# Performance work log

Hardware: AMD Instinct MI355X
Metric: run time of the kernel (lower is better)

Reference implementation:

```python
import jax, jax.numpy as jnp
import numpy as np

L, B, E = 2048, 4, 512      # seq len (= MoE group dim), batch (= MoE tokens-per-group), embed
H = 8                        # attention heads
FF = 2048                    # expert hidden dim
NE = 5                       # num experts
EPS = 1e-9
THRESHOLD = 0.2              # second_threshold_eval
CAP_FACTOR = 2.0             # capacity_factor_eval
MIN_CAP = 4
CAP = max(min(B, int(B * 2 * CAP_FACTOR / NE)), MIN_CAP)  # expert capacity per group


def setup_inputs() -> dict:
    key = jax.random.key(0)
    ks = jax.random.split(key, 8)
    s = lambda k, shape, scale: jax.random.normal(k, shape, jnp.float32) * scale
    return {
        "x": s(ks[0], (L, B, E), 1.0),
        "ln1_w": jnp.ones((E,), jnp.float32), "ln1_b": jnp.zeros((E,), jnp.float32),
        "ln2_w": jnp.ones((E,), jnp.float32), "ln2_b": jnp.zeros((E,), jnp.float32),
        "in_proj_w": s(ks[1], (3 * E, E), E ** -0.5), "in_proj_b": jnp.zeros((3 * E,), jnp.float32),
        "out_proj_w": s(ks[2], (E, E), E ** -0.5), "out_proj_b": jnp.zeros((E,), jnp.float32),
        "w_gating": s(ks[3], (E, NE), E ** -0.5),
        "w1": s(ks[4], (NE, E, FF), E ** -0.5),
        "w2": s(ks[5], (NE, FF, E), FF ** -0.5),
    }


def layer_norm(x, w, b, eps=1e-5):
    mu = x.mean(-1, keepdims=True)
    var = ((x - mu) ** 2).mean(-1, keepdims=True)
    return (x - mu) * jax.lax.rsqrt(var + eps) * w + b


def mha(x, wi, bi, wo, bo):
    # x: (L, B, E) as in torch nn.MultiheadAttention (batch_first=False)
    qkv = x @ wi.T + bi
    q, k, v = jnp.split(qkv, 3, axis=-1)
    hd = E // H
    q = q.reshape(L, B, H, hd) * (hd ** -0.5)
    k = k.reshape(L, B, H, hd)
    v = v.reshape(L, B, H, hd)
    scores = jnp.einsum('lbhd,mbhd->bhlm', q, k)          # (B,H,L,L)
    attn = jax.nn.softmax(scores, axis=-1)
    out = jnp.einsum('bhlm,mbhd->lbhd', attn, v).reshape(L, B, E)
    return out @ wo.T + bo


def top2_gating(x, w_gating, key):
    # x: (b=L, n=B, d); gshard-style top-2 gating, eval mode, 'random' second policy
    raw = jax.nn.softmax(x @ w_gating, axis=-1)            # (b,n,e)
    f32 = raw.dtype
    idx1 = jnp.argmax(raw, -1)
    gate1 = jnp.take_along_axis(raw, idx1[..., None], -1)[..., 0]
    m1 = jax.nn.one_hot(idx1, NE, dtype=f32)
    raw2 = raw * (1.0 - m1)
    idx2 = jnp.argmax(raw2, -1)
    gate2 = jnp.take_along_axis(raw2, idx2[..., None], -1)[..., 0]
    m2 = jax.nn.one_hot(idx2, NE, dtype=f32)
    denom = gate1 + gate2 + EPS
    gate1, gate2 = gate1 / denom, gate2 / denom
    # second_policy == 'random': keep second expert with prob gate2/threshold
    probs = jax.random.uniform(key, gate2.shape, f32)
    m2 = m2 * (probs < gate2 / THRESHOLD).astype(f32)[..., None]
    # capacity bookkeeping (exclusive cumsum over tokens, dim=-2)
    pos1 = (jnp.cumsum(m1, axis=-2) - m1) * m1
    m1 = m1 * (pos1 < CAP).astype(f32)
    m1_count = m1.sum(-2, keepdims=True)
    m1_flat = m1.sum(-1)
    pos1 = pos1.sum(-1)
    gate1 = gate1 * m1_flat
    pos2 = ((jnp.cumsum(m2, axis=-2) - m2) + m1_count) * m2
    m2 = m2 * (pos2 < CAP).astype(f32)
    m2_flat = m2.sum(-1)
    pos2 = pos2.sum(-1)
    gate2 = gate2 * m2_flat
    ohc = lambda p: jax.nn.one_hot(p.astype(jnp.int32), CAP, dtype=f32)  # safe: OOB -> zeros
    combine = (gate1[..., None, None] * m1_flat[..., None, None]
               * jax.nn.one_hot(idx1, NE, dtype=f32)[..., None] * ohc(pos1)[..., None, :]
               + gate2[..., None, None] * m2_flat[..., None, None]
               * jax.nn.one_hot(idx2, NE, dtype=f32)[..., None] * ohc(pos2)[..., None, :])
    dispatch = (combine != 0).astype(f32)
    return dispatch, combine


def moe(x, w_gating, w1, w2, key):
    dispatch, combine = top2_gating(x, w_gating, key)       # (b,n,e,c)
    ein = jnp.einsum('bnd,bnec->ebcd', x, dispatch)         # gather to experts
    h = jax.nn.relu(jnp.einsum('ebcd,edh->ebch', ein, w1))
    eo = jnp.einsum('ebch,ehd->ebcd', h, w2)
    return jnp.einsum('bnec,ebcd->bnd', combine, eo)        # scatter back


def reference(x, ln1_w, ln1_b, ln2_w, ln2_b, in_proj_w, in_proj_b,
              out_proj_w, out_proj_b, w_gating, w1, w2):
    key = jax.random.key(42)  # fixed RNG for 'random' second policy (eval determinism)
    h = layer_norm(x, ln1_w, ln1_b)
    x = x + mha(h, in_proj_w, in_proj_b, out_proj_w, out_proj_b)
    h2 = layer_norm(x, ln2_w, ln2_b)
    x = x + moe(h2, w_gating, w1, w2, key)
    return x
```

## Files before the change

### kernel.cpp

```cpp
#include <hip/hip_runtime.h>

#define DI __device__ __forceinline__

namespace {

constexpr int kL  = 2048;
constexpr int kB  = 4;
constexpr int kE  = 512;
constexpr int kHD = 64;
constexpr int kFF = 2048;
constexpr int kNE = 5;
constexpr int kT  = 8192;
constexpr int kCAP = 4;

using bf16x8 = __attribute__((ext_vector_type(8))) short;
using f32x4  = __attribute__((ext_vector_type(4))) float;

DI float bf2f(unsigned short u) { return __uint_as_float(((unsigned)u) << 16); }
DI unsigned short f2bf(float f) {
  unsigned u = __float_as_uint(f);
  u = u + 0x7FFFu + ((u >> 16) & 1u);
  return (unsigned short)(u >> 16);
}

DI unsigned rotl(unsigned v, int d) { return (v << d) | (v >> (32 - d)); }

DI void threefry(unsigned& x0, unsigned& x1) {
  const unsigned K1 = 0u, K2 = 42u, K3 = 0x1BD11BDAu ^ 0u ^ 42u;
  x0 += K1; x1 += K2;
  x0 += x1; x1 = rotl(x1, 13); x1 ^= x0;
  x0 += x1; x1 = rotl(x1, 15); x1 ^= x0;
  x0 += x1; x1 = rotl(x1, 26); x1 ^= x0;
  x0 += x1; x1 = rotl(x1,  6); x1 ^= x0;
  x0 += K2; x1 += K3 + 1u;
  x0 += x1; x1 = rotl(x1, 17); x1 ^= x0;
  x0 += x1; x1 = rotl(x1, 29); x1 ^= x0;
  x0 += x1; x1 = rotl(x1, 16); x1 ^= x0;
  x0 += x1; x1 = rotl(x1, 24); x1 ^= x0;
  x0 += K3; x1 += K1 + 2u;
  x0 += x1; x1 = rotl(x1, 13); x1 ^= x0;
  x0 += x1; x1 = rotl(x1, 15); x1 ^= x0;
  x0 += x1; x1 = rotl(x1, 26); x1 ^= x0;
  x0 += x1; x1 = rotl(x1,  6); x1 ^= x0;
  x0 += K1; x1 += K2 + 3u;
  x0 += x1; x1 = rotl(x1, 17); x1 ^= x0;
  x0 += x1; x1 = rotl(x1, 29); x1 ^= x0;
  x0 += x1; x1 = rotl(x1, 16); x1 ^= x0;
  x0 += x1; x1 = rotl(x1, 24); x1 ^= x0;
  x0 += K2; x1 += K3 + 4u;
  x0 += x1; x1 = rotl(x1, 13); x1 ^= x0;
  x0 += x1; x1 = rotl(x1, 15); x1 ^= x0;
  x0 += x1; x1 = rotl(x1, 26); x1 ^= x0;
  x0 += x1; x1 = rotl(x1,  6); x1 ^= x0;
  x0 += K3; x1 += K1 + 5u;
}

__global__ __launch_bounds__(256) void f2bf_kernel(
    const float* __restrict__ src, unsigned short* __restrict__ dst, int n4) {
  int i = blockIdx.x * blockDim.x + threadIdx.x;
  if (i >= n4) return;
  float4 v = ((const float4*)src)[i];
  ushort4 u;
  u.x = f2bf(v.x); u.y = f2bf(v.y); u.z = f2bf(v.z); u.w = f2bf(v.w);
  ((ushort4*)dst)[i] = u;
}

__global__ __launch_bounds__(256) void ln_kernel(
    const float* __restrict__ x, const float* __restrict__ w,
    const float* __restrict__ b, float* __restrict__ out) {
  int row = blockIdx.x;
  const float* xr = x + (size_t)row * kE;
  int t = threadIdx.x;
  float2 v = *(const float2*)(xr + t * 2);
  __shared__ float red[4];
  float s = v.x + v.y;
  #pragma unroll
  for (int m = 32; m; m >>= 1) s += __shfl_xor(s, m);
  if ((t & 63) == 0) red[t >> 6] = s;
  __syncthreads();
  float mu = (red[0] + red[1] + red[2] + red[3]) * (1.0f / kE);
  float dx = v.x - mu, dy = v.y - mu;
  float q = dx * dx + dy * dy;
  #pragma unroll
  for (int m = 32; m; m >>= 1) q += __shfl_xor(q, m);
  __syncthreads();
  if ((t & 63) == 0) red[t >> 6] = q;
  __syncthreads();
  float var = (red[0] + red[1] + red[2] + red[3]) * (1.0f / kE);
  float inv = 1.0f / sqrtf(var + 1e-5f);
  float2 o;
  o.x = dx * inv * w[t * 2]     + b[t * 2];
  o.y = dy * inv * w[t * 2 + 1] + b[t * 2 + 1];
  *(float2*)(out + (size_t)row * kE + t * 2) = o;
}

template <int BIAS, int RES, int SPLITOUT>
__global__ __launch_bounds__(256) void gemm_kernel(
    const float* __restrict__ Ap, const float* __restrict__ Bp,
    const float* __restrict__ biasp, const float* __restrict__ Rp,
    float* __restrict__ Cp, unsigned short* __restrict__ Chi,
    unsigned short* __restrict__ Clo, int M, int N, int K) {
  __shared__ float As[2][16][132];
  __shared__ float Bs[2][16][132];

  int nwg = gridDim.x * gridDim.y;
  int bid = blockIdx.y * gridDim.x + blockIdx.x;
  int swz = (bid & 7) * (nwg >> 3) + (bid >> 3);
  int wx = swz % gridDim.x, wy = swz / gridDim.x;

  const int m0 = wy * 128;
  const int n0 = wx * 128;
  const int t = threadIdx.x;
  const int tx = t & 15, ty = t >> 4;

  const int ar = t >> 2;
  const int ak = (t & 3) * 4;
  size_t arow0 = (size_t)(m0 + ar) * K + ak;
  size_t arow1 = (size_t)(m0 + ar + 64) * K + ak;
  const int b_r = t >> 2, b_o = (t & 3) * 4;

  float acc[8][8];
  #pragma unroll
  for (int i = 0; i < 8; ++i)
    #pragma unroll
    for (int j = 0; j < 8; ++j) acc[i][j] = 0.0f;

  float4 v0r, v1r, w0, w1v;
  auto load_tile = [&](int k0) {
    v0r = *(const float4*)(Ap + arow0 + k0);
    v1r = *(const float4*)(Ap + arow1 + k0);
    w0  = *(const float4*)(Bp + (size_t)(n0 + b_r) * K + k0 + b_o);
    w1v = *(const float4*)(Bp + (size_t)(n0 + b_r + 64) * K + k0 + b_o);
  };
  load_tile(0);

  for (int k0 = 0; k0 < K; k0 += 16) {
    const int bf = (k0 >> 4) & 1;
    As[bf][ak+0][ar] = v0r.x; As[bf][ak+1][ar] = v0r.y;
    As[bf][ak+2][ar] = v0r.z; As[bf][ak+3][ar] = v0r.w;
    As[bf][ak+0][ar+64] = v1r.x; As[bf][ak+1][ar+64] = v1r.y;
    As[bf][ak+2][ar+64] = v1r.z; As[bf][ak+3][ar+64] = v1r.w;
    Bs[bf][b_o+0][b_r] = w0.x; Bs[bf][b_o+1][b_r] = w0.y;
    Bs[bf][b_o+2][b_r] = w0.z; Bs[bf][b_o+3][b_r] = w0.w;
    Bs[bf][b_o+0][b_r+64] = w1v.x; Bs[bf][b_o+1][b_r+64] = w1v.y;
    Bs[bf][b_o+2][b_r+64] = w1v.z; Bs[bf][b_o+3][b_r+64] = w1v.w;
    __syncthreads();
    if (k0 + 16 < K) load_tile(k0 + 16);
    #pragma unroll
    for (int kk = 0; kk < 16; ++kk) {
      float av[8], bv[8];
      *(float4*)&av[0] = *(const float4*)&As[bf][kk][ty * 8];
      *(float4*)&av[4] = *(const float4*)&As[bf][kk][ty * 8 + 4];
      *(float4*)&bv[0] = *(const float4*)&Bs[bf][kk][tx * 4];
      *(float4*)&bv[4] = *(const float4*)&Bs[bf][kk][tx * 4 + 64];
      #pragma unroll
      for (int i = 0; i < 8; ++i)
        #pragma unroll
        for (int j = 0; j < 8; ++j)
          acc[i][j] = fmaf(av[i], bv[j], acc[i][j]);
    }
  }

  #pragma unroll
  for (int i = 0; i < 8; ++i) {
    int rloc = m0 + ty * 8 + i;
    size_t crow = (size_t)rloc * N;
    #pragma unroll
    for (int half = 0; half < 2; ++half) {
      int c = n0 + half * 64 + tx * 4;
      float v[4];
      #pragma unroll
      for (int j = 0; j < 4; ++j) {
        v[j] = acc[i][half * 4 + j];
        if (BIAS) v[j] += biasp[c + j];
        if (RES)  v[j] += Rp[crow + c + j];
      }
      if (SPLITOUT) {
        ushort4 hi4, lo4;
        unsigned short* hp = (unsigned short*)&hi4;
        unsigned short* lp = (unsigned short*)&lo4;
        #pragma unroll
        for (int j = 0; j < 4; ++j) {
          unsigned short hi = f2bf(v[j]);
          hp[j] = hi;
          lp[j] = f2bf(v[j] - bf2f(hi));
        }
        *(ushort4*)(Chi + crow + c) = hi4;
        *(ushort4*)(Clo + crow + c) = lo4;
      } else {
        *(float4*)(Cp + crow + c) = make_float4(v[0], v[1], v[2], v[3]);
      }
    }
  }
}

template <int GATHER, int RELU, int K, int N>
__global__ __launch_bounds__(256) void moe_mfma_kernel(
    const unsigned short* __restrict__ Abf, const unsigned short* __restrict__ Bbf,
    unsigned short* __restrict__ Cbf,
    const int* __restrict__ gatherp, const int* __restrict__ cntp,
    const int* __restrict__ basep) {
  __shared__ unsigned short As[128][40];
  __shared__ unsigned short Bs[128][40];

  const int e = blockIdx.z;
  const int M = cntp[e];
  const int rowOff = basep[e];
  if ((int)blockIdx.y * 128 >= M) return;
  const unsigned short* Bg = Bbf + (size_t)e * K * N;
  const int m0 = blockIdx.y * 128;
  const int n0 = blockIdx.x * 128;
  const int t = threadIdx.x;
  const int lane = t & 63, w = t >> 6;
  const int wm = w >> 1, wn = w & 1;

  const int ar = t >> 1, ah = t & 1;
  size_t abase;
  {
    int r = m0 + ar;
    int mm = M - 1; r = r < mm ? r : mm;
    if (GATHER) r = gatherp[rowOff + r];
    else        r += rowOff;
    abase = (size_t)r * K;
  }
  const int bk = t >> 3, bn = (t & 7) * 16;

  f32x4 acc[4][4];
  #pragma unroll
  for (int i = 0; i < 4; ++i)
    #pragma unroll
    for (int j = 0; j < 4; ++j)
      acc[i][j] = (f32x4){0.f, 0.f, 0.f, 0.f};

  uint4 aR0, aR1, bR0, bR1;
  auto gload = [&](int k0) {
    aR0 = *(const uint4*)(Abf + abase + k0 + ah * 16);
    aR1 = *(const uint4*)(Abf + abase + k0 + ah * 16 + 8);
    bR0 = *(const uint4*)(Bg + (size_t)(k0 + bk) * N + n0 + bn);
    bR1 = *(const uint4*)(Bg + (size_t)(k0 + bk) * N + n0 + bn + 8);
  };
  gload(0);

  const int kg = (lane >> 4) * 8;
  const int mr = lane & 15;

  for (int k0 = 0; k0 < K; k0 += 32) {
    __syncthreads();
    *(uint4*)&As[ar][ah * 16]     = aR0;
    *(uint4*)&As[ar][ah * 16 + 8] = aR1;
    {
      unsigned short tmp[16];
      *(uint4*)tmp       = bR0;
      *(uint4*)(tmp + 8) = bR1;
      #pragma unroll
      for (int j = 0; j < 16; ++j) Bs[bn + j][bk] = tmp[j];
    }
    __syncthreads();
    if (k0 + 32 < K) gload(k0 + 32);

    bf16x8 af[4], bfr[4];
    #pragma unroll
    for (int i = 0; i < 4; ++i)
      af[i] = *(const bf16x8*)&As[wm * 64 + i * 16 + mr][kg];
    #pragma unroll
    for (int j = 0; j < 4; ++j)
      bfr[j] = *(const bf16x8*)&Bs[wn * 64 + j * 16 + mr][kg];
    #pragma unroll
    for (int i = 0; i < 4; ++i)
      #pragma unroll
      for (int j = 0; j < 4; ++j)
        acc[i][j] = __builtin_amdgcn_mfma_f32_16x16x32_bf16(
            af[i], bfr[j], acc[i][j], 0, 0, 0);
  }

  const int lr4 = (lane >> 4) * 4;
  const int lc = lane & 15;
  #pragma unroll
  for (int i = 0; i < 4; ++i)
    #pragma unroll
    for (int r = 0; r < 4; ++r) {
      int row = m0 + wm * 64 + i * 16 + lr4 + r;
      if (row >= M) continue;
      size_t crow = (size_t)(row + rowOff) * N;
      #pragma unroll
      for (int j = 0; j < 4; ++j) {
        float v = acc[i][j][r];
        if (RELU) v = v > 0.f ? v : 0.f;
        Cbf[crow + n0 + wn * 64 + j * 16 + lc] = f2bf(v);
      }
    }
}

DI int pswz(int row) { return ((row >> 1) & 7) << 3; }

__global__ __launch_bounds__(256) void flash_kernel(
    const unsigned short* __restrict__ qh, const unsigned short* __restrict__ ql,
    float* __restrict__ attn_out) {
  __shared__ unsigned short KPhi[64][72];
  __shared__ unsigned short KPlo[64][72];
  __shared__ unsigned short Vthi[64][72];
  __shared__ unsigned short Vtlo[64][72];

  int bid = blockIdx.y * 32 + blockIdx.x;
  int swzb = (bid & 7) * 128 + (bid >> 3);
  const int bh = swzb >> 5;
  const int qt = swzb & 31;
  const int b = bh >> 3, h = bh & 7;
  const int t = threadIdx.x;
  const int w = t >> 6, lane = t & 63;
  const int l15 = lane & 15, l4 = lane >> 4;
  const int lr = t >> 2;
  const int dbase = (t & 3) * 16;
  const int vd = t & 63;
  const int kv0 = (t >> 6) * 16;

  bf16x8 qhi[2], qlo[2];
  {
    int qglob = qt * 64 + w * 16 + l15;
    size_t qoff = ((size_t)(qglob * kB + b)) * (3 * kE) + h * kHD;
    #pragma unroll
    for (int ks = 0; ks < 2; ++ks) {
      qhi[ks] = *(const bf16x8*)(qh + qoff + ks * 32 + l4 * 8);
      qlo[ks] = *(const bf16x8*)(ql + qoff + ks * 32 + l4 * 8);
    }
  }

  float m_i[4], l_i[4];
  f32x4 Oacc[4];
  #pragma unroll
  for (int r = 0; r < 4; ++r) { m_i[r] = -1e30f; l_i[r] = 0.f; }
  #pragma unroll
  for (int df = 0; df < 4; ++df) Oacc[df] = (f32x4){0.f, 0.f, 0.f, 0.f};

  uint4 kh[2], kl[2];
  unsigned short vh[16], vl[16];
  auto kv_load = [&](int ktile) {
    size_t koff = ((size_t)((ktile * 64 + lr) * kB + b)) * (3 * kE) + kE + h * kHD + dbase;
    kh[0] = *(const uint4*)(qh + koff);
    kh[1] = *(const uint4*)(qh + koff + 8);
    kl[0] = *(const uint4*)(ql + koff);
    kl[1] = *(const uint4*)(ql + koff + 8);
    #pragma unroll
    for (int j = 0; j < 16; ++j) {
      size_t voff = ((size_t)((ktile * 64 + kv0 + j) * kB + b)) * (3 * kE) + 2 * kE + h * kHD + vd;
      vh[j] = qh[voff];
      vl[j] = ql[voff];
    }
  };
  kv_load(0);

  for (int kt = 0; kt < 32; ++kt) {
    __syncthreads();
    {
      int sw = pswz(lr);
      *(uint4*)&KPhi[lr][(dbase)     ^ sw] = kh[0];
      *(uint4*)&KPhi[lr][(dbase + 8) ^ sw] = kh[1];
      *(uint4*)&KPlo[lr][(dbase)     ^ sw] = kl[0];
      *(uint4*)&KPlo[lr][(dbase + 8) ^ sw] = kl[1];
      int swv = pswz(vd);
      *(uint4*)&Vthi[vd][(kv0)     ^ swv] = ((uint4*)vh)[0];
      *(uint4*)&Vthi[vd][(kv0 + 8) ^ swv] = ((uint4*)vh)[1];
      *(uint4*)&Vtlo[vd][(kv0)     ^ swv] = ((uint4*)vl)[0];
      *(uint4*)&Vtlo[vd][(kv0 + 8) ^ swv] = ((uint4*)vl)[1];
    }
    __syncthreads();
    if (kt + 1 < 32) kv_load(kt + 1);

    f32x4 acc[4];
    #pragma unroll
    for (int nf = 0; nf < 4; ++nf) acc[nf] = (f32x4){0.f, 0.f, 0.f, 0.f};
    #pragma unroll
    for (int ks = 0; ks < 2; ++ks) {
      #pragma unroll
      for (int nf = 0; nf < 4; ++nf) {
        int krow = nf * 16 + l15;
        int off = (ks * 32 + l4 * 8) ^ pswz(krow);
        bf16x8 kkh = *(const bf16x8*)&KPhi[krow][off];
        bf16x8 kkl = *(const bf16x8*)&KPlo[krow][off];
        acc[nf] = __builtin_amdgcn_mfma_f32_16x16x32_bf16(qhi[ks], kkh, acc[nf], 0, 0, 0);
        acc[nf] = __builtin_amdgcn_mfma_f32_16x16x32_bf16(qhi[ks], kkl, acc[nf], 0, 0, 0);
        acc[nf] = __builtin_amdgcn_mfma_f32_16x16x32_bf16(qlo[ks], kkh, acc[nf], 0, 0, 0);
      }
    }
    #pragma unroll
    for (int nf = 0; nf < 4; ++nf)
      #pragma unroll
      for (int r = 0; r < 4; ++r) acc[nf][r] *= 0.125f;

    float pv[4][4];
    float alpha[4];
    #pragma unroll
    for (int r = 0; r < 4; ++r) {
      float tm = fmaxf(fmaxf(acc[0][r], acc[1][r]), fmaxf(acc[2][r], acc[3][r]));
      #pragma unroll
      for (int m = 1; m < 16; m <<= 1) tm = fmaxf(tm, __shfl_xor(tm, m));
      float mn = fmaxf(m_i[r], tm);
      alpha[r] = __expf(m_i[r] - mn);
      m_i[r] = mn;
      float rs = 0.f;
      #pragma unroll
      for (int nf = 0; nf < 4; ++nf) {
        float p = __expf(acc[nf][r] - mn);
        pv[r][nf] = p;
        rs += p;
      }
      #pragma unroll
      for (int m = 1; m < 16; m <<= 1) rs += __shfl_xor(rs, m);
      l_i[r] = l_i[r] * alpha[r] + rs;
    }
    #pragma unroll
    for (int df = 0; df < 4; ++df)
      #pragma unroll
      for (int r = 0; r < 4; ++r) Oacc[df][r] *= alpha[r];

    __syncthreads();
    #pragma unroll
    for (int r = 0; r < 4; ++r) {
      int qrow = w * 16 + l4 * 4 + r;
      int sw = pswz(qrow);
      #pragma unroll
      for (int nf = 0; nf < 4; ++nf) {
        int scol = (nf * 16 + l15) ^ sw;
        float p = pv[r][nf];
        unsigned short hi = f2bf(p);
        KPhi[qrow][scol] = hi;
        KPlo[qrow][scol] = f2bf(p - bf2f(hi));
      }
    }
    __syncthreads();

    {
      int prow = w * 16 + l15;
      int swp = pswz(prow);
      #pragma unroll
      for (int ks = 0; ks < 2; ++ks) {
        int koff = ks * 32 + l4 * 8;
        bf16x8 ph = *(const bf16x8*)&KPhi[prow][koff ^ swp];
        bf16x8 pl = *(const bf16x8*)&KPlo[prow][koff ^ swp];
        #pragma unroll
        for (int df = 0; df < 4; ++df) {
          int vrow = df * 16 + l15;
          int off = koff ^ pswz(vrow);
          bf16x8 vvh = *(const bf16x8*)&Vthi[vrow][off];
          bf16x8 vvl = *(const bf16x8*)&Vtlo[vrow][off];
          Oacc[df] = __builtin_amdgcn_mfma_f32_16x16x32_bf16(ph, vvh, Oacc[df], 0, 0, 0);
          Oacc[df] = __builtin_amdgcn_mfma_f32_16x16x32_bf16(ph, vvl, Oacc[df], 0, 0, 0);
          Oacc[df] = __builtin_amdgcn_mfma_f32_16x16x32_bf16(pl, vvh, Oacc[df], 0, 0, 0);
        }
      }
    }
  }

  #pragma unroll
  for (int r = 0; r < 4; ++r) {
    float inv = 1.0f / l_i[r];
    int l = qt * 64 + w * 16 + l4 * 4 + r;
    float* orow = attn_out + ((size_t)(l * kB + b)) * kE + h * kHD;
    #pragma unroll
    for (int df = 0; df < 4; ++df)
      orow[df * 16 + l15] = Oacc[df][r] * inv;
  }
}

__global__ __launch_bounds__(256) void gating_kernel(
    const float* __restrict__ h2, const float* __restrict__ wg,
    int* __restrict__ e1, int* __restrict__ e2,
    float* __restrict__ g1, float* __restrict__ g2,
    int* __restrict__ keepr) {
  __shared__ float swg[kE * kNE];
  for (int i = threadIdx.x; i < kE * kNE; i += 256) swg[i] = wg[i];
  __syncthreads();
  int w = threadIdx.x >> 6, lane = threadIdx.x & 63;
  int tok = blockIdx.x * 4 + w;
  const float* xr = h2 + (size_t)tok * kE;
  float a0=0,a1=0,a2=0,a3=0,a4=0;
  for (int d = lane; d < kE; d += 64) {
    float xv = xr[d];
    a0 = fmaf(xv, swg[d*5+0], a0);
    a1 = fmaf(xv, swg[d*5+1], a1);
    a2 = fmaf(xv, swg[d*5+2], a2);
    a3 = fmaf(xv, swg[d*5+3], a3);
    a4 = fmaf(xv, swg[d*5+4], a4);
  }
  #pragma unroll
  for (int m = 32; m; m >>= 1) {
    a0 += __shfl_xor(a0, m); a1 += __shfl_xor(a1, m); a2 += __shfl_xor(a2, m);
    a3 += __shfl_xor(a3, m); a4 += __shfl_xor(a4, m);
  }
  if (lane == 0) {
    float lg[5] = {a0, a1, a2, a3, a4};
    float mx = lg[0];
    #pragma unroll
    for (int e = 1; e < 5; ++e) mx = fmaxf(mx, lg[e]);
    float ex[5], ssum = 0.f;
    #pragma unroll
    for (int e = 0; e < 5; ++e) { ex[e] = expf(lg[e] - mx); ssum += ex[e]; }
    float raw[5];
    #pragma unroll
    for (int e = 0; e < 5; ++e) raw[e] = ex[e] / ssum;
    int i1 = 0; float v1 = raw[0];
    #pragma unroll
    for (int e = 1; e < 5; ++e) if (raw[e] > v1) { v1 = raw[e]; i1 = e; }
    int i2 = 0; float v2 = -1.f;
    #pragma unroll
    for (int e = 0; e < 5; ++e) if (e != i1 && raw[e] > v2) { v2 = raw[e]; i2 = e; }
    float denom = v1 + v2 + 1e-9f;
    float G1 = v1 / denom, G2 = v2 / denom;
    unsigned x0 = 0u, x1 = (unsigned)tok;
    threefry(x0, x1);
    unsigned bits = x0 ^ x1;
    float u = __uint_as_float((bits >> 9) | 0x3F800000u) - 1.0f;
    int kr = (u < G2 / 0.2f) ? 1 : 0;
    e1[tok] = i1; e2[tok] = i2; g1[tok] = G1; g2[tok] = G2; keepr[tok] = kr;
  }
}

__global__ __launch_bounds__(256) void plan_kernel(
    const int* __restrict__ e1, const int* __restrict__ e2,
    const int* __restrict__ keepr,
    int* __restrict__ slot1, int* __restrict__ slot2, int* __restrict__ tot) {
  int l = blockIdx.x * blockDim.x + threadIdx.x;
  if (l >= kL) return;
  int base = l * 4;
  int e1v[4], e2v[4], kr[4];
  #pragma unroll
  for (int n = 0; n < 4; ++n) {
    e1v[n] = e1[base + n]; e2v[n] = e2[base + n]; kr[n] = keepr[base + n];
  }
  int c1[5] = {0,0,0,0,0};
  int s1[4];
  #pragma unroll
  for (int n = 0; n < 4; ++n) {
    int e = e1v[n];
    int p = 0;
    #pragma unroll
    for (int q = 0; q < 5; ++q) if (q == e) p = c1[q];
    s1[n] = p;
    #pragma unroll
    for (int q = 0; q < 5; ++q) c1[q] += (q == e);
  }
  int run[5] = {0,0,0,0,0};
  int s2[4];
  #pragma unroll
  for (int n = 0; n < 4; ++n) {
    s2[n] = -1;
    if (kr[n]) {
      int e = e2v[n];
      int p = 0;
      #pragma unroll
      for (int q = 0; q < 5; ++q) if (q == e) p = c1[q] + run[q];
      if (p < kCAP) s2[n] = p;
      #pragma unroll
      for (int q = 0; q < 5; ++q) run[q] += (q == e);
    }
  }
  #pragma unroll
  for (int n = 0; n < 4; ++n) { slot1[base + n] = s1[n]; slot2[base + n] = s2[n]; }
  int adm[5] = {0,0,0,0,0};
  #pragma unroll
  for (int n = 0; n < 4; ++n)
    if (s2[n] >= 0) {
      #pragma unroll
      for (int q = 0; q < 5; ++q) adm[q] += (q == e2v[n]);
    }
  #pragma unroll
  for (int q = 0; q < 5; ++q) tot[l * kNE + q] = c1[q] + adm[q];
}

__global__ __launch_bounds__(256) void scan_kernel(
    const int* __restrict__ tot, int* __restrict__ gbase, int* __restrict__ cnt) {
  int e = blockIdx.x;
  int t = threadIdx.x;
  int lane = t & 63, w = t >> 6;
  __shared__ int wsum[4];
  __shared__ int carry;
  if (t == 0) carry = 0;
  __syncthreads();
  for (int chunk = 0; chunk < kL / 256; ++chunk) {
    int g = chunk * 256 + t;
    int v = tot[g * kNE + e];
    int inc = v;
    #pragma unroll
    for (int off = 1; off < 64; off <<= 1) {
      int u = __shfl_up(inc, off);
      if (lane >= off) inc += u;
    }
    if (lane == 63) wsum[w] = inc;
    __syncthreads();
    int wb = 0;
    #pragma unroll
    for (int i = 0; i < 4; ++i) wb += (i < w) ? wsum[i] : 0;
    int total = wsum[0] + wsum[1] + wsum[2] + wsum[3];
    gbase[g * kNE + e] = carry + wb + inc - v;
    __syncthreads();
    if (t == 0) carry += total;
    __syncthreads();
  }
  if (t == 0) cnt[e] = carry;
}

__global__ void bases_kernel(const int* __restrict__ cnt, int* __restrict__ base) {
  if (threadIdx.x == 0 && blockIdx.x == 0) {
    int a = 0;
    #pragma unroll
    for (int e = 0; e < kNE; ++e) { base[e] = a; a += cnt[e]; }
  }
}

__global__ __launch_bounds__(256) void rowmap_kernel(
    const int* __restrict__ e1, const int* __restrict__ e2,
    const int* __restrict__ slot1, const int* __restrict__ slot2,
    const int* __restrict__ gbase, const int* __restrict__ ebase,
    int* __restrict__ rowOf1, int* __restrict__ rowOf2,
    int* __restrict__ tokOfRow) {
  int tok = blockIdx.x * blockDim.x + threadIdx.x;
  if (tok >= kT) return;
  int l = tok >> 2;
  int a = e1[tok];
  int r1 = ebase[a] + gbase[l * kNE + a] + slot1[tok];
  rowOf1[tok] = r1;
  tokOfRow[r1] = tok;
  int s2 = slot2[tok];
  int r2 = -1;
  if (s2 >= 0) {
    int bq = e2[tok];
    r2 = ebase[bq] + gbase[l * kNE + bq] + s2;
    tokOfRow[r2] = tok;
  }
  rowOf2[tok] = r2;
}

__global__ __launch_bounds__(128) void combine_kernel(
    const float* __restrict__ xres, const unsigned short* __restrict__ eo,
    const float* __restrict__ g1, const float* __restrict__ g2,
    const int* __restrict__ rowOf1, const int* __restrict__ rowOf2,
    float* __restrict__ out) {
  int tok = blockIdx.x;
  int t = threadIdx.x;
  float4 o = *(const float4*)(xres + (size_t)tok * kE + t * 4);
  int p1 = rowOf1[tok];
  float G1 = g1[tok];
  ushort4 a = *(const ushort4*)(eo + (size_t)p1 * kE + t * 4);
  o.x += G1 * bf2f(a.x); o.y += G1 * bf2f(a.y);
  o.z += G1 * bf2f(a.z); o.w += G1 * bf2f(a.w);
  int p2 = rowOf2[tok];
  if (p2 >= 0) {
    float G2 = g2[tok];
    ushort4 c = *(const ushort4*)(eo + (size_t)p2 * kE + t * 4);
    o.x += G2 * bf2f(c.x); o.y += G2 * bf2f(c.y);
    o.z += G2 * bf2f(c.z); o.w += G2 * bf2f(c.w);
  }
  *(float4*)(out + (size_t)tok * kE + t * 4) = o;
}

}

extern "C" void kernel_launch(void* const* d_in, const int* in_sizes, int n_in,
                              void* d_out, int out_size, void* d_ws, size_t ws_size,
                              hipStream_t stream) {
  (void)in_sizes; (void)n_in; (void)out_size;
  const float* x    = (const float*)d_in[0];
  const float* ln1w = (const float*)d_in[1];
  const float* ln1b = (const float*)d_in[2];
  const float* ln2w = (const float*)d_in[3];
  const float* ln2b = (const float*)d_in[4];
  const float* wqkv = (const float*)d_in[5];
  const float* bqkv = (const float*)d_in[6];
  const float* wo   = (const float*)d_in[7];
  const float* bo   = (const float*)d_in[8];
  const float* wg   = (const float*)d_in[9];
  const float* w1   = (const float*)d_in[10];
  const float* w2   = (const float*)d_in[11];
  float* out = (float*)d_out;

  if (ws_size < (size_t)135000000) return;
  float* ws   = (float*)d_ws;
  float* xres = ws;
  unsigned short* qkvhi = (unsigned short*)(ws + 4194304);
  unsigned short* qkvlo = (unsigned short*)(ws + 10485760);
  unsigned short* hmoe  = (unsigned short*)(ws + 4194304);
  float* h1   = ws + 16777216;
  float* h2   = ws + 20971520;
  unsigned short* eobf = (unsigned short*)(ws + 20971520);
  unsigned short* h2bf = (unsigned short*)(ws + 25165824);
  unsigned short* w1bf = (unsigned short*)(ws + 27262976);
  unsigned short* w2bf = (unsigned short*)(ws + 29884416);
  int* ibuf    = (int*)(ws + 32505856);
  int* e1      = ibuf;
  int* e2      = e1 + kT;
  float* g1f   = (float*)(e2 + kT);
  float* g2f   = g1f + kT;
  int* keepr   = (int*)(g2f + kT);
  int* slot1   = keepr + kT;
  int* slot2   = slot1 + kT;
  int* rowOf1  = slot2 + kT;
  int* rowOf2  = rowOf1 + kT;
  int* tot     = rowOf2 + kT;
  int* gbase   = tot + kL * kNE;
  int* tokOfRow= gbase + kL * kNE;
  int* cnt     = tokOfRow + 2 * kT;
  int* ebase   = cnt + 8;

  f2bf_kernel<<<5120, 256, 0, stream>>>(w1, w1bf, kNE * kE * kFF / 4);
  f2bf_kernel<<<5120, 256, 0, stream>>>(w2, w2bf, kNE * kFF * kE / 4);
  ln_kernel<<<kT, 256, 0, stream>>>(x, ln1w, ln1b, h1);
  gemm_kernel<1,0,1><<<dim3(12, 64, 1), 256, 0, stream>>>(
      h1, wqkv, bqkv, nullptr, nullptr, qkvhi, qkvlo, kT, 1536, kE);
  flash_kernel<<<dim3(32, 32, 1), 256, 0, stream>>>(qkvhi, qkvlo, h1);
  gemm_kernel<1,1,0><<<dim3(4, 64, 1), 256, 0, stream>>>(
      h1, wo, bo, x, xres, nullptr, nullptr, kT, kE, kE);
  ln_kernel<<<kT, 256, 0, stream>>>(xres, ln2w, ln2b, h2);
  gating_kernel<<<kL, 256, 0, stream>>>(h2, wg, e1, e2, g1f, g2f, keepr);
  f2bf_kernel<<<4096, 256, 0, stream>>>(h2, h2bf, kT * kE / 4);
  plan_kernel<<<kL / 256, 256, 0, stream>>>(e1, e2, keepr, slot1, slot2, tot);
  scan_kernel<<<kNE, 256, 0, stream>>>(tot, gbase, cnt);
  bases_kernel<<<1, 32, 0, stream>>>(cnt, ebase);
  rowmap_kernel<<<kT / 256, 256, 0, stream>>>(
      e1, e2, slot1, slot2, gbase, ebase, rowOf1, rowOf2, tokOfRow);
  moe_mfma_kernel<1,1,kE,kFF><<<dim3(16, 64, kNE), 256, 0, stream>>>(
      h2bf, w1bf, hmoe, tokOfRow, cnt, ebase);
  moe_mfma_kernel<0,0,kFF,kE><<<dim3(4, 64, kNE), 256, 0, stream>>>(
      hmoe, w2bf, eobf, nullptr, cnt, ebase);
  combine_kernel<<<kT, 128, 0, stream>>>(
      xres, eobf, g1f, g2f, rowOf1, rowOf2, out);
}
```

Baseline: 762.3 us.

## Replace FP32 SIMT attention projections with split-bf16 MFMA GEMMs

Swaps the FP32 FMA-based GEMM used for the QKV and output projections for an MFMA kernel that splits each operand into bf16 hi/lo parts and accumulates three products (hi*hi, hi*lo, lo*hi) to approximate FP32 accuracy. LayerNorm and the flash attention epilogue now emit hi/lo bf16 pairs directly, and the projection weights are split once per call by a new kernel. The goal is to move the dense projection math onto matrix cores. The cost is extra split passes over the weights, more memory traffic for the two-part activations, and some loss of precision. The workspace layout is reorganised to hold the new buffers.

```diff
diff --git a/kernel.cpp b/kernel.cpp
--- a/kernel.cpp
+++ b/kernel.cpp
@@ -65,9 +65,31 @@
   ((ushort4*)dst)[i] = u;
 }
 
+__global__ __launch_bounds__(256) void wsplit_kernel(
+    const float* __restrict__ src, unsigned short* __restrict__ hi,
+    unsigned short* __restrict__ lo, int n4) {
+  int i = blockIdx.x * blockDim.x + threadIdx.x;
+  if (i >= n4) return;
+  float4 v = ((const float4*)src)[i];
+  float va[4] = {v.x, v.y, v.z, v.w};
+  ushort4 h4, l4;
+  unsigned short* hp = (unsigned short*)&h4;
+  unsigned short* lp = (unsigned short*)&l4;
+  #pragma unroll
+  for (int j = 0; j < 4; ++j) {
+    unsigned short h = f2bf(va[j]);
+    hp[j] = h;
+    lp[j] = f2bf(va[j] - bf2f(h));
+  }
+  ((ushort4*)hi)[i] = h4;
+  ((ushort4*)lo)[i] = l4;
+}
+
+template <int SPLIT>
 __global__ __launch_bounds__(256) void ln_kernel(
     const float* __restrict__ x, const float* __restrict__ w,
-    const float* __restrict__ b, float* __restrict__ out) {
+    const float* __restrict__ b, float* __restrict__ out,
+    unsigned short* __restrict__ ohi, unsigned short* __restrict__ olo) {
   int row = blockIdx.x;
   const float* xr = x + (size_t)row * kE;
   int t = threadIdx.x;
@@ -88,110 +110,119 @@
   __syncthreads();
   float var = (red[0] + red[1] + red[2] + red[3]) * (1.0f / kE);
   float inv = 1.0f / sqrtf(var + 1e-5f);
-  float2 o;
-  o.x = dx * inv * w[t * 2]     + b[t * 2];
-  o.y = dy * inv * w[t * 2 + 1] + b[t * 2 + 1];
-  *(float2*)(out + (size_t)row * kE + t * 2) = o;
-}
-
-template <int BIAS, int RES, int SPLITOUT>
-__global__ __launch_bounds__(256) void gemm_kernel(
-    const float* __restrict__ Ap, const float* __restrict__ Bp,
+  float ox = dx * inv * w[t * 2]     + b[t * 2];
+  float oy = dy * inv * w[t * 2 + 1] + b[t * 2 + 1];
+  if (SPLIT) {
+    size_t base = (size_t)row * kE + t * 2;
+    unsigned short hx = f2bf(ox), hy = f2bf(oy);
+    ohi[base] = hx; ohi[base + 1] = hy;
+    olo[base] = f2bf(ox - bf2f(hx)); olo[base + 1] = f2bf(oy - bf2f(hy));
+  } else {
+    *(float2*)(out + (size_t)row * kE + t * 2) = make_float2(ox, oy);
+  }
+}
+
+template <int RES, int SPLITOUT>
+__global__ __launch_bounds__(256) void dsgemm_kernel(
+    const unsigned short* __restrict__ Ahi, const unsigned short* __restrict__ Alo,
+    const unsigned short* __restrict__ Bhi, const unsigned short* __restrict__ Blo,
     const float* __restrict__ biasp, const float* __restrict__ Rp,
-    float* __restrict__ Cp, unsigned short* __restrict__ Chi,
+    float* __restrict__ Cf, unsigned short* __restrict__ Chi,
     unsigned short* __restrict__ Clo, int M, int N, int K) {
-  __shared__ float As[2][16][132];
-  __shared__ float Bs[2][16][132];
+  __shared__ unsigned short AHs[128][40];
+  __shared__ unsigned short ALs[128][40];
+  __shared__ unsigned short BHs[128][40];
+  __shared__ unsigned short BLs[128][40];
 
   int nwg = gridDim.x * gridDim.y;
   int bid = blockIdx.y * gridDim.x + blockIdx.x;
   int swz = (bid & 7) * (nwg >> 3) + (bid >> 3);
   int wx = swz % gridDim.x, wy = swz / gridDim.x;
-
   const int m0 = wy * 128;
   const int n0 = wx * 128;
+
   const int t = threadIdx.x;
-  const int tx = t & 15, ty = t >> 4;
-
-  const int ar = t >> 2;
-  const int ak = (t & 3) * 4;
-  size_t arow0 = (size_t)(m0 + ar) * K + ak;
-  size_t arow1 = (size_t)(m0 + ar + 64) * K + ak;
-  const int b_r = t >> 2, b_o = (t & 3) * 4;
-
-  float acc[8][8];
-  #pragma unroll
-  for (int i = 0; i < 8; ++i)
-    #pragma unroll
-    for (int j = 0; j < 8; ++j) acc[i][j] = 0.0f;
-
-  float4 v0r, v1r, w0, w1v;
-  auto load_tile = [&](int k0) {
-    v0r = *(const float4*)(Ap + arow0 + k0);
-    v1r = *(const float4*)(Ap + arow1 + k0);
-    w0  = *(const float4*)(Bp + (size_t)(n0 + b_r) * K + k0 + b_o);
-    w1v = *(const float4*)(Bp + (size_t)(n0 + b_r + 64) * K + k0 + b_o);
+  const int lane = t & 63, w = t >> 6;
+  const int wm = w >> 1, wn = w & 1;
+  const int ar = t >> 1, ah = t & 1;
+
+  f32x4 acc[4][4];
+  #pragma unroll
+  for (int i = 0; i < 4; ++i)
+    #pragma unroll
+    for (int j = 0; j < 4; ++j)
+      acc[i][j] = (f32x4){0.f, 0.f, 0.f, 0.f};
+
+  uint4 aH[2], aL[2], bH[2], bL[2];
+  auto gload = [&](int k0) {
+    size_t aoff = (size_t)(m0 + ar) * K + k0 + ah * 16;
+    aH[0] = *(const uint4*)(Ahi + aoff); aH[1] = *(const uint4*)(Ahi + aoff + 8);
+    aL[0] = *(const uint4*)(Alo + aoff); aL[1] = *(const uint4*)(Alo + aoff + 8);
+    size_t boff = (size_t)(n0 + ar) * K + k0 + ah * 16;
+    bH[0] = *(const uint4*)(Bhi + boff); bH[1] = *(const uint4*)(Bhi + boff + 8);
+    bL[0] = *(const uint4*)(Blo + boff); bL[1] = *(const uint4*)(Blo + boff + 8);
   };
-  load_tile(0);
-
-  for (int k0 = 0; k0 < K; k0 += 16) {
-    const int bf = (k0 >> 4) & 1;
-    As[bf][ak+0][ar] = v0r.x; As[bf][ak+1][ar] = v0r.y;
-    As[bf][ak+2][ar] = v0r.z; As[bf][ak+3][ar] = v0r.w;
-    As[bf][ak+0][ar+64] = v1r.x; As[bf][ak+1][ar+64] = v1r.y;
-    As[bf][ak+2][ar+64] = v1r.z; As[bf][ak+3][ar+64] = v1r.w;
-    Bs[bf][b_o+0][b_r] = w0.x; Bs[bf][b_o+1][b_r] = w0.y;
-    Bs[bf][b_o+2][b_r] = w0.z; Bs[bf][b_o+3][b_r] = w0.w;
-    Bs[bf][b_o+0][b_r+64] = w1v.x; Bs[bf][b_o+1][b_r+64] = w1v.y;
-    Bs[bf][b_o+2][b_r+64] = w1v.z; Bs[bf][b_o+3][b_r+64] = w1v.w;
-    __syncthreads();
-    if (k0 + 16 < K) load_tile(k0 + 16);
-    #pragma unroll
-    for (int kk = 0; kk < 16; ++kk) {
-      float av[8], bv[8];
-      *(float4*)&av[0] = *(const float4*)&As[bf][kk][ty * 8];
-      *(float4*)&av[4] = *(const float4*)&As[bf][kk][ty * 8 + 4];
-      *(float4*)&bv[0] = *(const float4*)&Bs[bf][kk][tx * 4];
-      *(float4*)&bv[4] = *(const float4*)&Bs[bf][kk][tx * 4 + 64];
-      #pragma unroll
-      for (int i = 0; i < 8; ++i)
-        #pragma unroll
-        for (int j = 0; j < 8; ++j)
-          acc[i][j] = fmaf(av[i], bv[j], acc[i][j]);
-    }
-  }
-
-  #pragma unroll
-  for (int i = 0; i < 8; ++i) {
-    int rloc = m0 + ty * 8 + i;
-    size_t crow = (size_t)rloc * N;
-    #pragma unroll
-    for (int half = 0; half < 2; ++half) {
-      int c = n0 + half * 64 + tx * 4;
-      float v[4];
+  gload(0);
+
+  const int kg = (lane >> 4) * 8;
+  const int mr = lane & 15;
+
+  for (int k0 = 0; k0 < K; k0 += 32) {
+    __syncthreads();
+    *(uint4*)&AHs[ar][ah * 16]     = aH[0];
+    *(uint4*)&AHs[ar][ah * 16 + 8] = aH[1];
+    *(uint4*)&ALs[ar][ah * 16]     = aL[0];
+    *(uint4*)&ALs[ar][ah * 16 + 8] = aL[1];
+    *(uint4*)&BHs[ar][ah * 16]     = bH[0];
+    *(uint4*)&BHs[ar][ah * 16 + 8] = bH[1];
+    *(uint4*)&BLs[ar][ah * 16]     = bL[0];
+    *(uint4*)&BLs[ar][ah * 16 + 8] = bL[1];
+    __syncthreads();
+    if (k0 + 32 < K) gload(k0 + 32);
+
+    bf16x8 afH[4], afL[4], bfH[4], bfL[4];
+    #pragma unroll
+    for (int i = 0; i < 4; ++i) {
+      afH[i] = *(const bf16x8*)&AHs[wm * 64 + i * 16 + mr][kg];
+      afL[i] = *(const bf16x8*)&ALs[wm * 64 + i * 16 + mr][kg];
+    }
+    #pragma unroll
+    for (int j = 0; j < 4; ++j) {
+      bfH[j] = *(const bf16x8*)&BHs[wn * 64 + j * 16 + mr][kg];
+      bfL[j] = *(const bf16x8*)&BLs[wn * 64 + j * 16 + mr][kg];
+    }
+    #pragma unroll
+    for (int i = 0; i < 4; ++i)
       #pragma unroll
       for (int j = 0; j < 4; ++j) {
-        v[j] = acc[i][half * 4 + j];
-        if (BIAS) v[j] += biasp[c + j];
-        if (RES)  v[j] += Rp[crow + c + j];
+        acc[i][j] = __builtin_amdgcn_mfma_f32_16x16x32_bf16(afH[i], bfH[j], acc[i][j], 0, 0, 0);
+        acc[i][j] = __builtin_amdgcn_mfma_f32_16x16x32_bf16(afH[i], bfL[j], acc[i][j], 0, 0, 0);
+        acc[i][j] = __builtin_amdgcn_mfma_f32_16x16x32_bf16(afL[i], bfH[j], acc[i][j], 0, 0, 0);
       }
-      if (SPLITOUT) {
-        ushort4 hi4, lo4;
-        unsigned short* hp = (unsigned short*)&hi4;
-        unsigned short* lp = (unsigned short*)&lo4;
-        #pragma unroll
-        for (int j = 0; j < 4; ++j) {
-          unsigned short hi = f2bf(v[j]);
-          hp[j] = hi;
-          lp[j] = f2bf(v[j] - bf2f(hi));
+  }
+
+  const int lr4 = (lane >> 4) * 4;
+  const int lc = lane & 15;
+  #pragma unroll
+  for (int i = 0; i < 4; ++i)
+    #pragma unroll
+    for (int r = 0; r < 4; ++r) {
+      int row = m0 + wm * 64 + i * 16 + lr4 + r;
+      size_t crow = (size_t)row * N;
+      #pragma unroll
+      for (int j = 0; j < 4; ++j) {
+        int col = n0 + wn * 64 + j * 16 + lc;
+        float v = acc[i][j][r] + biasp[col];
+        if (RES) v += Rp[crow + col];
+        if (SPLITOUT) {
+          unsigned short hi = f2bf(v);
+          Chi[crow + col] = hi;
+          Clo[crow + col] = f2bf(v - bf2f(hi));
+        } else {
+          Cf[crow + col] = v;
         }
-        *(ushort4*)(Chi + crow + c) = hi4;
-        *(ushort4*)(Clo + crow + c) = lo4;
-      } else {
-        *(float4*)(Cp + crow + c) = make_float4(v[0], v[1], v[2], v[3]);
       }
     }
-  }
 }
 
 template <int GATHER, int RELU, int K, int N>
@@ -295,7 +326,7 @@
 
 __global__ __launch_bounds__(256) void flash_kernel(
     const unsigned short* __restrict__ qh, const unsigned short* __restrict__ ql,
-    float* __restrict__ attn_out) {
+    unsigned short* __restrict__ aohi, unsigned short* __restrict__ aolo) {
   __shared__ unsigned short KPhi[64][72];
   __shared__ unsigned short KPlo[64][72];
   __shared__ unsigned short Vthi[64][72];
@@ -455,10 +486,14 @@
   for (int r = 0; r < 4; ++r) {
     float inv = 1.0f / l_i[r];
     int l = qt * 64 + w * 16 + l4 * 4 + r;
-    float* orow = attn_out + ((size_t)(l * kB + b)) * kE + h * kHD;
-    #pragma unroll
-    for (int df = 0; df < 4; ++df)
-      orow[df * 16 + l15] = Oacc[df][r] * inv;
+    size_t obase = ((size_t)(l * kB + b)) * kE + h * kHD;
+    #pragma unroll
+    for (int df = 0; df < 4; ++df) {
+      float o = Oacc[df][r] * inv;
+      unsigned short hi = f2bf(o);
+      aohi[obase + df * 16 + l15] = hi;
+      aolo[obase + df * 16 + l15] = f2bf(o - bf2f(hi));
+    }
   }
 }
 
@@ -673,19 +708,27 @@
   const float* w2   = (const float*)d_in[11];
   float* out = (float*)d_out;
 
-  if (ws_size < (size_t)135000000) return;
+  if (ws_size < (size_t)134742016) return;
   float* ws   = (float*)d_ws;
   float* xres = ws;
-  unsigned short* qkvhi = (unsigned short*)(ws + 4194304);
-  unsigned short* qkvlo = (unsigned short*)(ws + 10485760);
-  unsigned short* hmoe  = (unsigned short*)(ws + 4194304);
-  float* h1   = ws + 16777216;
-  float* h2   = ws + 20971520;
-  unsigned short* eobf = (unsigned short*)(ws + 20971520);
-  unsigned short* h2bf = (unsigned short*)(ws + 25165824);
-  unsigned short* w1bf = (unsigned short*)(ws + 27262976);
-  unsigned short* w2bf = (unsigned short*)(ws + 29884416);
-  int* ibuf    = (int*)(ws + 32505856);
+  unsigned short* w1bf   = (unsigned short*)(ws + 4194304);
+  unsigned short* w2bf   = (unsigned short*)(ws + 6815744);
+  unsigned short* wqkvhi = (unsigned short*)(ws + 9437184);
+  unsigned short* wqkvlo = (unsigned short*)(ws + 9830400);
+  unsigned short* wohi   = (unsigned short*)(ws + 10223616);
+  unsigned short* wolo   = (unsigned short*)(ws + 10354688);
+  int* ibuf = (int*)(ws + 10485760);
+  unsigned short* h1hi  = (unsigned short*)(ws + 10616832);
+  unsigned short* h1lo  = (unsigned short*)(ws + 12713984);
+  unsigned short* qkvhi = (unsigned short*)(ws + 14811136);
+  unsigned short* qkvlo = (unsigned short*)(ws + 21102592);
+  unsigned short* aohi  = (unsigned short*)(ws + 27394048);
+  unsigned short* aolo  = (unsigned short*)(ws + 29491200);
+  float* h2             = ws + 10616832;
+  unsigned short* eobf  = (unsigned short*)(ws + 10616832);
+  unsigned short* h2bf  = (unsigned short*)(ws + 14811136);
+  unsigned short* hmoe  = (unsigned short*)(ws + 16908288);
+
   int* e1      = ibuf;
   int* e2      = e1 + kT;
   float* g1f   = (float*)(e2 + kT);
@@ -703,13 +746,17 @@
 
   f2bf_kernel<<<5120, 256, 0, stream>>>(w1, w1bf, kNE * kE * kFF / 4);
   f2bf_kernel<<<5120, 256, 0, stream>>>(w2, w2bf, kNE * kFF * kE / 4);
-  ln_kernel<<<kT, 256, 0, stream>>>(x, ln1w, ln1b, h1);
-  gemm_kernel<1,0,1><<<dim3(12, 64, 1), 256, 0, stream>>>(
-      h1, wqkv, bqkv, nullptr, nullptr, qkvhi, qkvlo, kT, 1536, kE);
-  flash_kernel<<<dim3(32, 32, 1), 256, 0, stream>>>(qkvhi, qkvlo, h1);
-  gemm_kernel<1,1,0><<<dim3(4, 64, 1), 256, 0, stream>>>(
-      h1, wo, bo, x, xres, nullptr, nullptr, kT, kE, kE);
-  ln_kernel<<<kT, 256, 0, stream>>>(xres, ln2w, ln2b, h2);
+  wsplit_kernel<<<768, 256, 0, stream>>>(wqkv, wqkvhi, wqkvlo, 1536 * kE / 4);
+  wsplit_kernel<<<256, 256, 0, stream>>>(wo, wohi, wolo, kE * kE / 4);
+  ln_kernel<1><<<kT, 256, 0, stream>>>(x, ln1w, ln1b, nullptr, h1hi, h1lo);
+  dsgemm_kernel<0,1><<<dim3(12, 64), 256, 0, stream>>>(
+      h1hi, h1lo, wqkvhi, wqkvlo, bqkv, nullptr,
+      nullptr, qkvhi, qkvlo, kT, 1536, kE);
+  flash_kernel<<<dim3(32, 32, 1), 256, 0, stream>>>(qkvhi, qkvlo, aohi, aolo);
+  dsgemm_kernel<1,0><<<dim3(4, 64), 256, 0, stream>>>(
+      aohi, aolo, wohi, wolo, bo, x,
+      xres, nullptr, nullptr, kT, kE, kE);
+  ln_kernel<0><<<kT, 256, 0, stream>>>(xres, ln2w, ln2b, h2, nullptr, nullptr);
   gating_kernel<<<kL, 256, 0, stream>>>(h2, wg, e1, e2, g1f, g2f, keepr);
   f2bf_kernel<<<4096, 256, 0, stream>>>(h2, h2bf, kT * kE / 4);
   plan_kernel<<<kL / 256, 256, 0, stream>>>(e1, e2, keepr, slot1, slot2, tot);
```

Result: faster. 719.3 us (-5.6%).
